# Performance work log

Hardware: AMD Instinct MI355X
Metric: run time of the kernel (lower is better)

Reference implementation:

```python
import jax, jax.numpy as jnp
import numpy as np

N_NODES = 200000
N_EDGES = 800000
N_GRAPHS = 4096
IN_FEAT = 64
CONV_SIZES = [128, 128, 256, 256]
MAX_DEGREE = 5  # buckets 0..5 (degree clamped)
N_CLASSES = 2


def setup_inputs() -> dict:
    key = jax.random.key(0)
    ks = jax.random.split(key, 32)
    inp = {}
    inp["x"] = jax.random.normal(ks[0], (N_NODES, IN_FEAT), dtype=jnp.float32)
    inp["edge_index"] = jax.random.randint(ks[1], (2, N_EDGES), 0, N_NODES, dtype=jnp.int32)
    inp["batch"] = jnp.sort(jax.random.randint(ks[2], (N_NODES,), 0, N_GRAPHS, dtype=jnp.int32))
    # per-layer MFConv params: Wl (neighbor-sum branch, with bias), Wr (root branch, no bias),
    # one linear per degree bucket -> leading dim MAX_DEGREE+1
    c_in = IN_FEAT
    k = 3
    for li, c_out in enumerate(CONV_SIZES):
        s = 1.0 / np.sqrt(c_in)
        inp[f"Wl{li}"] = jax.random.normal(ks[k], (MAX_DEGREE + 1, c_in, c_out), dtype=jnp.float32) * s; k += 1
        inp[f"bl{li}"] = jax.random.normal(ks[k], (MAX_DEGREE + 1, c_out), dtype=jnp.float32) * 0.01; k += 1
        inp[f"Wr{li}"] = jax.random.normal(ks[k], (MAX_DEGREE + 1, c_in, c_out), dtype=jnp.float32) * s; k += 1
        c_in = c_out
    in_final = sum(CONV_SIZES) + CONV_SIZES[-1]  # concat of all layer outputs + pooled last layer
    inp["Wf"] = jax.random.normal(ks[k], (in_final, N_CLASSES), dtype=jnp.float32) * (1.0 / np.sqrt(in_final)); k += 1
    inp["bf"] = jax.random.normal(ks[k], (N_CLASSES,), dtype=jnp.float32) * 0.01
    return inp


def _mfconv(x, src, dst, deg, Wl, bl, Wr):
    # neighbor sum aggregation (source_to_target flow): msg_i = sum_{j->i} x_j
    msg = jax.ops.segment_sum(x[src], dst, num_segments=x.shape[0])  # [N, c_in]
    out = jnp.zeros((x.shape[0], Wl.shape[2]), dtype=x.dtype)
    for d in range(Wl.shape[0]):  # small fixed loop over degree buckets
        r = msg @ Wl[d] + bl[d] + x @ Wr[d]
        out = jnp.where((deg == d)[:, None], r, out)
    return out


def reference(x, edge_index, batch,
              Wl0, bl0, Wr0, Wl1, bl1, Wr1, Wl2, bl2, Wr2, Wl3, bl3, Wr3,
              Wf, bf):
    src, dst = edge_index[0], edge_index[1]
    n = x.shape[0]
    deg = jnp.clip(jnp.zeros((n,), jnp.int32).at[dst].add(1), 0, MAX_DEGREE)
    hs = []
    h = x
    for Wl, bl, Wr in ((Wl0, bl0, Wr0), (Wl1, bl1, Wr1), (Wl2, bl2, Wr2), (Wl3, bl3, Wr3)):
        h = _mfconv(h, src, dst, deg, Wl, bl, Wr)
        hs.append(h)
    # global_add_pool then repeat_interleave back to nodes == gather pooled by batch id
    h_pool = jax.ops.segment_sum(h, batch, num_segments=N_GRAPHS)  # [G, c_last]
    h_pool_ = h_pool[batch]  # [N, c_last]
    h_cat = jnp.concatenate(hs + [h_pool_], axis=1)  # [N, sum(sizes)+c_last]
    logits = h_cat @ Wf + bf
    return jax.nn.softmax(logits, axis=1)
```

## Files before the change

### kernel.cpp

```cpp
#include <hip/hip_runtime.h>
#include <cstdint>
#include <cstddef>

namespace {

constexpr int NN   = 200000;
constexpr int NE   = 800000;
constexpr int NG   = 4096;
constexpr int MAXD = 5;

constexpr int BM = 64;
constexpr int KT = 32;
constexpr int NBC = (NN + 255) / 256;
constexpr int NBLK  = (NN + BM - 1) / BM + 6;
constexpr int PERMN = NBLK * BM;

typedef _Float16 half8 __attribute__((ext_vector_type(8)));
typedef _Float16 half4 __attribute__((ext_vector_type(4)));
typedef float    f32x4 __attribute__((ext_vector_type(4)));

constexpr size_t P_L0 = (size_t)6 * 128 * 128;
constexpr size_t P_L1 = (size_t)6 * 256 * 128;
constexpr size_t P_L2 = (size_t)6 * 256 * 256;
constexpr size_t P_L3 = (size_t)6 * 512 * 256;
constexpr size_t O_P0 = 0;
constexpr size_t O_P1 = O_P0 + P_L0;
constexpr size_t O_P2 = O_P1 + P_L1;
constexpr size_t O_P3 = O_P2 + P_L2;
constexpr size_t WTOT = O_P3 + P_L3;


__global__ void k_memset32(int* __restrict__ p, int v, int n) {
    int i = blockIdx.x * 256 + threadIdx.x;
    if (i < n) p[i] = v;
}

__global__ void k_report(float* __restrict__ outp, float v, int n) {
    int i = blockIdx.x * 256 + threadIdx.x;
    if (i < n) outp[i] = v;
}

template <int CIN, int COUT>
__global__ void k_wpack(const float* __restrict__ Wl, const float* __restrict__ Wr,
                        _Float16* __restrict__ hi, _Float16* __restrict__ lo) {
    constexpr int NT = CIN / 16;
    constexpr int NB = COUT / 16;
    const int total = 6 * NT * NB * 64;
    int idx = blockIdx.x * 256 + threadIdx.x;
    if (idx >= total) return;
    const int lane = idx & 63;
    int rest = idx >> 6;
    const int nb = rest % NB; rest /= NB;
    const int ti = rest % NT;
    const int d  = rest / NT;
    const int k0 = ti * 32 + ((lane >> 4) * 8);
    const int n  = nb * 16 + (lane & 15);
    half8 hv, lv;
#pragma unroll
    for (int j = 0; j < 8; j++) {
        const int kk = k0 + j;
        const float v = (kk < CIN)
                            ? Wl[((size_t)d * CIN + kk) * COUT + n]
                            : Wr[((size_t)d * CIN + (kk - CIN)) * COUT + n];
        const _Float16 h = (_Float16)v;
        hv[j] = h;
        lv[j] = (_Float16)(v - (float)h);
    }
    *(half8*)(hi + (size_t)idx * 8) = hv;
    *(half8*)(lo + (size_t)idx * 8) = lv;
}


__global__ void k_count_deg(const int* __restrict__ dst, int* __restrict__ deg) {
    int e = blockIdx.x * 256 + threadIdx.x;
    if (e < NE) atomicAdd(&deg[dst[e]], 1);
}

__global__ void k_scan_part(const int* __restrict__ deg, int* __restrict__ part) {
    __shared__ int s[256];
    int t = threadIdx.x, i = blockIdx.x * 256 + t;
    s[t] = (i < NN) ? deg[i] : 0;
    __syncthreads();
    for (int st = 128; st > 0; st >>= 1) {
        if (t < st) s[t] += s[t + st];
        __syncthreads();
    }
    if (t == 0) part[blockIdx.x] = s[0];
}

__global__ void k_scan_single(int* __restrict__ part, int nb) {
    __shared__ int s[1024];
    int t = threadIdx.x;
    int v0 = (t < nb) ? part[t] : 0;
    s[t] = v0;
    __syncthreads();
    for (int off = 1; off < 1024; off <<= 1) {
        int v = (t >= off) ? s[t - off] : 0;
        __syncthreads();
        s[t] += v;
        __syncthreads();
    }
    if (t < nb) part[t] = s[t] - v0;
}

__global__ void k_scan_final(const int* __restrict__ deg, const int* __restrict__ part,
                             int* __restrict__ row_ptr, int* __restrict__ cursor) {
    __shared__ int s[256];
    int t = threadIdx.x, i = blockIdx.x * 256 + t;
    int v0 = (i < NN) ? deg[i] : 0;
    s[t] = v0;
    __syncthreads();
    for (int off = 1; off < 256; off <<= 1) {
        int v = (t >= off) ? s[t - off] : 0;
        __syncthreads();
        s[t] += v;
        __syncthreads();
    }
    if (i < NN) {
        int excl = s[t] - v0 + part[blockIdx.x];
        row_ptr[i] = excl;
        cursor[i]  = excl;
        if (i == NN - 1) row_ptr[NN] = excl + v0;
    }
}

__global__ void k_fill_csr(const int* __restrict__ src, const int* __restrict__ dst,
                           int* __restrict__ cursor, int* __restrict__ col) {
    int e = blockIdx.x * 256 + threadIdx.x;
    if (e < NE) {
        int d = dst[e];
        int slot = atomicAdd(&cursor[d], 1);
        col[slot] = src[e];
    }
}


__global__ void k_bucket_blockcount(const int* __restrict__ deg, int* __restrict__ blkcnt) {
    __shared__ int h[6];
    int t = threadIdx.x;
    if (t < 6) h[t] = 0;
    __syncthreads();
    int i = blockIdx.x * 256 + t;
    if (i < NN) atomicAdd(&h[min(deg[i], MAXD)], 1);
    __syncthreads();
    if (t < 6) blkcnt[t * NBC + blockIdx.x] = h[t];
}

__global__ void k_bucket_scanall(int* __restrict__ blkcnt, int* __restrict__ bpad) {
    __shared__ int tot[6];
    int t = threadIdx.x;
    if (t < 6) {
        int run = 0;
        for (int j = 0; j < NBC; j++) {
            int v = blkcnt[t * NBC + j];
            blkcnt[t * NBC + j] = run;
            run += v;
        }
        tot[t] = run;
    }
    __syncthreads();
    if (t == 0) {
        int off = 0;
        for (int b = 0; b < 6; b++) {
            bpad[b] = off;
            off += ((tot[b] + BM - 1) / BM) * BM;
        }
        bpad[6] = off;
    }
}

__global__ void k_scatter2(const int* __restrict__ deg, const int* __restrict__ blkcnt,
                           const int* __restrict__ bpad, int* __restrict__ perm) {
    __shared__ int base[6];
    int t = threadIdx.x;
    if (t < 6) base[t] = bpad[t] + blkcnt[t * NBC + blockIdx.x];
    __syncthreads();
    int i = blockIdx.x * 256 + t;
    if (i < NN) {
        int b = min(deg[i], MAXD);
        int pos = atomicAdd(&base[b], 1);
        perm[pos] = i;
    }
}


__global__ void k_aggregate128(const float* __restrict__ hin, const int* __restrict__ row_ptr,
                               const int* __restrict__ col, float* __restrict__ msg) {
    int node = blockIdx.x * 4 + (threadIdx.x >> 6);
    int lane = threadIdx.x & 63;
    int s = row_ptr[node], e = row_ptr[node + 1];
    float2 acc = make_float2(0.f, 0.f);
    for (int p = s; p < e; p++) {
        const float2 v = *(const float2*)(hin + (size_t)col[p] * 128 + lane * 2);
        acc.x += v.x; acc.y += v.y;
    }
    *(float2*)(msg + (size_t)node * 128 + lane * 2) = acc;
}


template <int C0, int C1, int COUT, int BN_, bool POOL_FUSE>
__launch_bounds__(256, (BN_ == 256) ? 3 : 4)
__global__ void k_transform(const float* __restrict__ hin0, const float* __restrict__ hin1,
                            const int* __restrict__ row_ptr, const int* __restrict__ col,
                            const _Float16* __restrict__ wph, const _Float16* __restrict__ wpl,
                            const float* __restrict__ bias, const float* __restrict__ Wf,
                            const int* __restrict__ perm, const int* __restrict__ deg,
                            const int* __restrict__ batch,
                            float* __restrict__ out0, float* __restrict__ pool,
                            float* __restrict__ logits, int wf_off) {
    constexpr int CIN = C0 + C1;
    constexpr int NW0 = C0 / 32;
    constexpr int NW  = CIN / 32;
    constexpr int NT  = 2 * NW;
    constexpr int NB  = COUT / 16;
    constexpr int NTN = BN_ / 64;
    __shared__ _Float16 Ah[4][64][8];
    __shared__ _Float16 Al[4][64][8];
    __shared__ int rowid[BM];

    const int t  = threadIdx.x;
    const int m0 = blockIdx.x * BM;
    const int n0 = blockIdx.y * BN_;

    if (t < BM) rowid[t] = perm[m0 + t];
    __syncthreads();
    if (rowid[0] < 0) return;

    const int d = min(deg[rowid[0]], MAXD);

    const int am = t & 63, aq = t >> 6;
    const int anode = rowid[am];
    int es = 0, ee = 0;
    if (anode >= 0) { es = row_ptr[anode]; ee = row_ptr[anode + 1]; }
    const int lx = t & 15, qd = (t >> 4) & 3, wv = t >> 6;

    const int mt_w = am >> 4;
    const int lA1  = (am & 15) + ((aq >> 1) << 4);
    const int lA2  = (am & 15) + ((2 + (aq >> 1)) << 4);
    const int j0   = (aq & 1) * 4;

    const int nb0 = n0 / 16 + wv * NTN;

    auto gather = [&](int ti, float* g) {
#pragma unroll
        for (int i = 0; i < 8; i++) g[i] = 0.f;
        if (ti < NW) {
            const bool lo = (C1 == 0) || (ti < NW0);
            const float* base = lo ? hin0 : hin1;
            const int stride  = lo ? C0 : C1;
            const int off     = (lo ? 32 * ti : 32 * (ti - NW0)) + 4 * aq;
            for (int p = es; p < ee; p++) {
                const float* r = base + (size_t)col[p] * stride + off;
                const float4 a = *(const float4*)r;
                const float4 b = *(const float4*)(r + 16);
                g[0] += a.x; g[1] += a.y; g[2] += a.z; g[3] += a.w;
                g[4] += b.x; g[5] += b.y; g[6] += b.z; g[7] += b.w;
            }
        } else if (anode >= 0) {
            const int e = (ti - NW) * 32 + 4 * aq;
            const float* r = (C1 == 0 || e < C0)
                                 ? hin0 + (size_t)anode * C0 + e
                                 : hin1 + (size_t)anode * C1 + (e - C0);
            const float4 a = *(const float4*)r;
            const float4 b = *(const float4*)(r + 16);
            g[0] = a.x; g[1] = a.y; g[2] = a.z; g[3] = a.w;
            g[4] = b.x; g[5] = b.y; g[6] = b.z; g[7] = b.w;
        }
    };

    f32x4 acc[4][NTN];
#pragma unroll
    for (int mt = 0; mt < 4; mt++)
#pragma unroll
        for (int nt = 0; nt < NTN; nt++) acc[mt][nt] = (f32x4)0.f;

    float gcur[8];
    gather(0, gcur);

    for (int ti = 0; ti < NT; ti++) {
        {
            half4 h1, l1, h2, l2;
#pragma unroll
            for (int i = 0; i < 4; i++) {
                const _Float16 h = (_Float16)gcur[i];
                h1[i] = h; l1[i] = (_Float16)(gcur[i] - (float)h);
                const _Float16 g = (_Float16)gcur[4 + i];
                h2[i] = g; l2[i] = (_Float16)(gcur[4 + i] - (float)g);
            }
            *(half4*)&Ah[mt_w][lA1][j0] = h1;
            *(half4*)&Al[mt_w][lA1][j0] = l1;
            *(half4*)&Ah[mt_w][lA2][j0] = h2;
            *(half4*)&Al[mt_w][lA2][j0] = l2;
        }
        half8 bh[NTN], bl[NTN];
        {
            const size_t tbase = (((size_t)d * NT + ti) * NB) * 512;
#pragma unroll
            for (int nt = 0; nt < NTN; nt++) {
                const size_t off = tbase + (size_t)(nb0 + nt) * 512 + (size_t)am * 8;
                bh[nt] = *(const half8*)(wph + off);
                bl[nt] = *(const half8*)(wpl + off);
            }
        }
        __syncthreads();

        float gnext[8];
        if (ti + 1 < NT) {
            gather(ti + 1, gnext);
        } else {
#pragma unroll
            for (int i = 0; i < 8; i++) gnext[i] = 0.f;
        }

        {
            half8 ah[4], alo[4];
#pragma unroll
            for (int mt = 0; mt < 4; mt++) {
                ah[mt]  = *(const half8*)&Ah[mt][am][0];
                alo[mt] = *(const half8*)&Al[mt][am][0];
            }
#pragma unroll
            for (int nt = 0; nt < NTN; nt++)
#pragma unroll
                for (int mt = 0; mt < 4; mt++) {
                    acc[mt][nt] = __builtin_amdgcn_mfma_f32_16x16x32_f16(ah[mt],  bh[nt], acc[mt][nt], 0, 0, 0);
                    acc[mt][nt] = __builtin_amdgcn_mfma_f32_16x16x32_f16(alo[mt], bh[nt], acc[mt][nt], 0, 0, 0);
                    acc[mt][nt] = __builtin_amdgcn_mfma_f32_16x16x32_f16(ah[mt],  bl[nt], acc[mt][nt], 0, 0, 0);
                }
        }
        __syncthreads();

#pragma unroll
        for (int i = 0; i < 8; i++) gcur[i] = gnext[i];
    }

    float blv[NTN], w0[NTN], w1[NTN];
    int cols[NTN];
#pragma unroll
    for (int nt = 0; nt < NTN; nt++) {
        cols[nt] = n0 + wv * (16 * NTN) + nt * 16 + lx;
        blv[nt] = bias[d * COUT + cols[nt]];
        w0[nt]  = Wf[(size_t)(wf_off + cols[nt]) * 2 + 0];
        w1[nt]  = Wf[(size_t)(wf_off + cols[nt]) * 2 + 1];
    }
#pragma unroll
    for (int mt = 0; mt < 4; mt++)
#pragma unroll
    for (int r = 0; r < 4; r++) {
        const int node = rowid[mt * 16 + qd * 4 + r];
        float p0 = 0.f, p1 = 0.f;
        if (node >= 0) {
            float h[NTN];
#pragma unroll
            for (int nt = 0; nt < NTN; nt++) {
                h[nt] = acc[mt][nt][r] + blv[nt];
                p0 = fmaf(h[nt], w0[nt], p0);
                p1 = fmaf(h[nt], w1[nt], p1);
            }
            if constexpr (POOL_FUSE) {
                float* pr = pool + (size_t)batch[node] * 256;
#pragma unroll
                for (int nt = 0; nt < NTN; nt++) atomicAdd(&pr[cols[nt]], h[nt]);
            } else {
                float* orow = out0 + (size_t)node * COUT;
#pragma unroll
                for (int nt = 0; nt < NTN; nt++) orow[cols[nt]] = h[nt];
            }
        }
#pragma unroll
        for (int s = 1; s < 16; s <<= 1) {
            p0 += __shfl_xor(p0, s, 64);
            p1 += __shfl_xor(p1, s, 64);
        }
        if (node >= 0 && lx == 0) {
            atomicAdd(&logits[(size_t)node * 2 + 0], p0);
            atomicAdd(&logits[(size_t)node * 2 + 1], p1);
        }
    }
}


__launch_bounds__(256, 3)
__global__ void k_gemm2b(float* __restrict__ buf0, float* __restrict__ buf1,
                         const _Float16* __restrict__ wph, const _Float16* __restrict__ wpl,
                         const float* __restrict__ bias, const float* __restrict__ Wf,
                         const int* __restrict__ perm, const int* __restrict__ deg,
                         float* __restrict__ logits) {
    constexpr int COUT = 256, NT = 8, NB = 16, NTN = 4;
    __shared__ _Float16 Ah[4][64][8];
    __shared__ _Float16 Al[4][64][8];
    __shared__ int rowid[BM];

    const int t  = threadIdx.x;
    const int m0 = blockIdx.x * BM;

    if (t < BM) rowid[t] = perm[m0 + t];
    __syncthreads();
    if (rowid[0] < 0) return;

    const int d = min(deg[rowid[0]], MAXD);

    const int am = t & 63, aq = t >> 6;
    const int anode = rowid[am];
    const int lx = t & 15, qd = (t >> 4) & 3, wv = t >> 6;

    const int mt_w = am >> 4;
    const int lA1  = (am & 15) + ((aq >> 1) << 4);
    const int lA2  = (am & 15) + ((2 + (aq >> 1)) << 4);
    const int j0   = (aq & 1) * 4;
    const int nb0  = wv * NTN;

    f32x4 acc[4][NTN];
#pragma unroll
    for (int mt = 0; mt < 4; mt++)
#pragma unroll
        for (int nt = 0; nt < NTN; nt++) acc[mt][nt] = (f32x4)0.f;

    for (int ti = 0; ti < NT; ti++) {
        {
            const int gk0 = ti * 32 + 4 * aq;
            float4 v0 = make_float4(0.f, 0.f, 0.f, 0.f);
            float4 v1 = v0;
            if (anode >= 0) {
                const float* r = (gk0 < 128) ? buf0 + (size_t)anode * 128 + gk0
                                             : buf1 + (size_t)anode * 128 + (gk0 - 128);
                v0 = *(const float4*)r;
                v1 = *(const float4*)(r + 16);
            }
            const float g[8] = {v0.x, v0.y, v0.z, v0.w, v1.x, v1.y, v1.z, v1.w};
            half4 h1, l1, h2, l2;
#pragma unroll
            for (int i = 0; i < 4; i++) {
                const _Float16 h = (_Float16)g[i];
                h1[i] = h; l1[i] = (_Float16)(g[i] - (float)h);
                const _Float16 q = (_Float16)g[4 + i];
                h2[i] = q; l2[i] = (_Float16)(g[4 + i] - (float)q);
            }
            *(half4*)&Ah[mt_w][lA1][j0] = h1;
            *(half4*)&Al[mt_w][lA1][j0] = l1;
            *(half4*)&Ah[mt_w][lA2][j0] = h2;
            *(half4*)&Al[mt_w][lA2][j0] = l2;
        }
        half8 bh[NTN], bl[NTN];
        {
            const size_t tbase = (((size_t)d * NT + ti) * NB) * 512;
#pragma unroll
            for (int nt = 0; nt < NTN; nt++) {
                const size_t off = tbase + (size_t)(nb0 + nt) * 512 + (size_t)am * 8;
                bh[nt] = *(const half8*)(wph + off);
                bl[nt] = *(const half8*)(wpl + off);
            }
        }
        __syncthreads();
        {
            half8 ah[4], alo[4];
#pragma unroll
            for (int mt = 0; mt < 4; mt++) {
                ah[mt]  = *(const half8*)&Ah[mt][am][0];
                alo[mt] = *(const half8*)&Al[mt][am][0];
            }
#pragma unroll
            for (int nt = 0; nt < NTN; nt++)
#pragma unroll
                for (int mt = 0; mt < 4; mt++) {
                    acc[mt][nt] = __builtin_amdgcn_mfma_f32_16x16x32_f16(ah[mt],  bh[nt], acc[mt][nt], 0, 0, 0);
                    acc[mt][nt] = __builtin_amdgcn_mfma_f32_16x16x32_f16(alo[mt], bh[nt], acc[mt][nt], 0, 0, 0);
                    acc[mt][nt] = __builtin_amdgcn_mfma_f32_16x16x32_f16(ah[mt],  bl[nt], acc[mt][nt], 0, 0, 0);
                }
        }
        __syncthreads();
    }

    float blv[NTN], w0[NTN], w1[NTN];
    int cols[NTN];
#pragma unroll
    for (int nt = 0; nt < NTN; nt++) {
        cols[nt] = wv * 64 + nt * 16 + lx;
        blv[nt] = bias[d * COUT + cols[nt]];
        w0[nt]  = Wf[(size_t)(256 + cols[nt]) * 2 + 0];
        w1[nt]  = Wf[(size_t)(256 + cols[nt]) * 2 + 1];
    }
#pragma unroll
    for (int mt = 0; mt < 4; mt++)
#pragma unroll
    for (int r = 0; r < 4; r++) {
        const int node = rowid[mt * 16 + qd * 4 + r];
        float p0 = 0.f, p1 = 0.f;
        if (node >= 0) {
#pragma unroll
            for (int nt = 0; nt < NTN; nt++) {
                const float h = acc[mt][nt][r] + blv[nt];
                p0 = fmaf(h, w0[nt], p0);
                p1 = fmaf(h, w1[nt], p1);
                if (cols[nt] < 128) buf0[(size_t)node * 128 + cols[nt]] = h;
                else                buf1[(size_t)node * 128 + cols[nt] - 128] = h;
            }
        }
#pragma unroll
        for (int s = 1; s < 16; s <<= 1) {
            p0 += __shfl_xor(p0, s, 64);
            p1 += __shfl_xor(p1, s, 64);
        }
        if (node >= 0 && lx == 0) {
            atomicAdd(&logits[(size_t)node * 2 + 0], p0);
            atomicAdd(&logits[(size_t)node * 2 + 1], p1);
        }
    }
}


__global__ void k_pool_logits(const float* __restrict__ pool, const float* __restrict__ Wf,
                              const float* __restrict__ bf, float* __restrict__ pl) {
    int g = blockIdx.x * 4 + (threadIdx.x >> 6);
    int lane = threadIdx.x & 63;
    const float* pr = pool + (size_t)g * 256;
    float p0 = 0.f, p1 = 0.f;
#pragma unroll
    for (int j = 0; j < 4; j++) {
        int k = lane + 64 * j;
        float v = pr[k];
        p0 = fmaf(v, Wf[(size_t)(768 + k) * 2 + 0], p0);
        p1 = fmaf(v, Wf[(size_t)(768 + k) * 2 + 1], p1);
    }
#pragma unroll
    for (int s = 1; s < 64; s <<= 1) {
        p0 += __shfl_xor(p0, s, 64);
        p1 += __shfl_xor(p1, s, 64);
    }
    if (lane == 0) {
        pl[(size_t)g * 2 + 0] = p0 + bf[0];
        pl[(size_t)g * 2 + 1] = p1 + bf[1];
    }
}

__global__ void k_final(const float* __restrict__ logits, const float* __restrict__ pl,
                        const int* __restrict__ batch, float* __restrict__ outp) {
    int i = blockIdx.x * 256 + threadIdx.x;
    if (i < NN) {
        int g = batch[i];
        float l0 = logits[(size_t)i * 2 + 0] + pl[(size_t)g * 2 + 0];
        float l1 = logits[(size_t)i * 2 + 1] + pl[(size_t)g * 2 + 1];
        float m = fmaxf(l0, l1);
        float e0 = expf(l0 - m), e1 = expf(l1 - m);
        float inv = 1.f / (e0 + e1);
        outp[(size_t)i * 2 + 0] = e0 * inv;
        outp[(size_t)i * 2 + 1] = e1 * inv;
    }
}

}

extern "C" void kernel_launch(void* const* d_in, const int* in_sizes, int n_in,
                              void* d_out, int out_size, void* d_ws, size_t ws_size,
                              hipStream_t stream) {
    const float* x     = (const float*)d_in[0];
    const int*   ei    = (const int*)d_in[1];
    const int*   batch = (const int*)d_in[2];
    const float* Wl0 = (const float*)d_in[3];  const float* bl0 = (const float*)d_in[4];
    const float* Wr0 = (const float*)d_in[5];
    const float* Wl1 = (const float*)d_in[6];  const float* bl1 = (const float*)d_in[7];
    const float* Wr1 = (const float*)d_in[8];
    const float* Wl2 = (const float*)d_in[9];  const float* bl2 = (const float*)d_in[10];
    const float* Wr2 = (const float*)d_in[11];
    const float* Wl3 = (const float*)d_in[12]; const float* bl3 = (const float*)d_in[13];
    const float* Wr3 = (const float*)d_in[14];
    const float* Wf  = (const float*)d_in[15]; const float* bf  = (const float*)d_in[16];
    const int* src = ei;
    const int* dst = ei + NE;
    float* outp = (float*)d_out;
    (void)in_sizes; (void)n_in;

    char* w = (char*)d_ws;
    auto alloc = [&](size_t bytes) -> void* {
        void* p = (void*)w;
        w += (bytes + 255) & ~(size_t)255;
        return p;
    };
    int*   deg    = (int*)alloc((size_t)NN * 4);
    float* logits = (float*)alloc((size_t)NN * 2 * 4);
    float* pool   = (float*)alloc((size_t)NG * 256 * 4);
    size_t zero_words = (size_t)(w - (char*)deg) / 4;
    int*   bpad    = (int*)alloc(32);
    int*   blkcnt  = (int*)alloc((size_t)6 * NBC * 4);
    int*   perm    = (int*)alloc((size_t)PERMN * 4);
    int*   row_ptr = (int*)alloc((size_t)(NN + 1) * 4);
    int*   cursor  = (int*)alloc((size_t)NN * 4);
    int*   col     = (int*)alloc((size_t)NE * 4);
    int*   part    = (int*)alloc(1024 * 4);
    float* pl      = (float*)alloc((size_t)NG * 2 * 4);
    _Float16* whi  = (_Float16*)alloc(WTOT * 2);
    _Float16* wlo  = (_Float16*)alloc(WTOT * 2);
    float* bufA    = (float*)alloc((size_t)NN * 128 * 4);
    float* bufB    = (float*)alloc((size_t)NN * 128 * 4);

    size_t required = (size_t)(w - (char*)d_ws);
    if (required > ws_size) {
        k_report<<<(out_size + 255) / 256, 256, 0, stream>>>(
            outp, (float)(double)(ws_size >> 20), out_size);
        return;
    }

    dim3 b256(256);
    k_memset32<<<(int)((zero_words + 255) / 256), b256, 0, stream>>>((int*)deg, 0, (int)zero_words);
    k_memset32<<<(PERMN + 255) / 256, b256, 0, stream>>>(perm, -1, PERMN);

    k_wpack<64, 128><<<(int)(P_L0 / 8 + 255) / 256, b256, 0, stream>>>(Wl0, Wr0, whi + O_P0, wlo + O_P0);
    k_wpack<128, 128><<<(int)(P_L1 / 8 + 255) / 256, b256, 0, stream>>>(Wl1, Wr1, whi + O_P1, wlo + O_P1);
    k_wpack<128, 256><<<(int)(P_L2 / 8 + 255) / 256, b256, 0, stream>>>(Wl2, Wr2, whi + O_P2, wlo + O_P2);
    k_wpack<256, 256><<<(int)(P_L3 / 8 + 255) / 256, b256, 0, stream>>>(Wl3, Wr3, whi + O_P3, wlo + O_P3);

    k_count_deg<<<NE / 256, b256, 0, stream>>>(dst, deg);
    k_scan_part<<<NBC, b256, 0, stream>>>(deg, part);
    k_scan_single<<<1, 1024, 0, stream>>>(part, NBC);
    k_scan_final<<<NBC, b256, 0, stream>>>(deg, part, row_ptr, cursor);
    k_fill_csr<<<NE / 256, b256, 0, stream>>>(src, dst, cursor, col);
    k_bucket_blockcount<<<NBC, b256, 0, stream>>>(deg, blkcnt);
    k_bucket_scanall<<<1, 64, 0, stream>>>(blkcnt, bpad);
    k_scatter2<<<NBC, b256, 0, stream>>>(deg, blkcnt, bpad, perm);

    k_transform<64, 0, 128, 128, false><<<dim3(NBLK, 1), b256, 0, stream>>>(
        x, nullptr, row_ptr, col, whi + O_P0, wlo + O_P0,
        bl0, Wf, perm, deg, nullptr, bufA, nullptr, logits, 0);
    k_transform<128, 0, 128, 128, false><<<dim3(NBLK, 1), b256, 0, stream>>>(
        bufA, nullptr, row_ptr, col, whi + O_P1, wlo + O_P1,
        bl1, Wf, perm, deg, nullptr, bufB, nullptr, logits, 128);
    k_aggregate128<<<NN / 4, b256, 0, stream>>>(bufB, row_ptr, col, bufA);
    k_gemm2b<<<dim3(NBLK), b256, 0, stream>>>(
        bufA, bufB, whi + O_P2, wlo + O_P2, bl2, Wf, perm, deg, logits);
    k_transform<128, 128, 256, 256, true><<<dim3(NBLK, 1), b256, 0, stream>>>(
        bufA, bufB, row_ptr, col, whi + O_P3, wlo + O_P3,
        bl3, Wf, perm, deg, batch, nullptr, pool, logits, 512);

    k_pool_logits<<<NG / 4, b256, 0, stream>>>(pool, Wf, bf, pl);
    k_final<<<NBC, b256, 0, stream>>>(logits, pl, batch, outp);
}
```

Measured before the change: 1.486 ms.

## Stage full gathered A tile in LDS once and load root rows directly

The transform kernels now gather and sum the neighbor features for the whole input width in a single pass, each thread covering a contiguous quarter of the channels. The result is split into hi/lo fp16 and written into a full-K LDS tile behind one barrier, replacing the per-k-tile gather plus two syncs per iteration. The root-branch operand is read straight from global memory into MFMA register layout, with no LDS staging. The neighbor aggregation kernel is unrolled by two edges, and launch bounds drop to fewer waves per SIMD to make room for the larger LDS footprint and register use. The trade is lower occupancy and more LDS in exchange for fewer barriers and more memory-level parallelism in the gather.

```diff
diff --git a/kernel.cpp b/kernel.cpp
--- a/kernel.cpp
+++ b/kernel.cpp
@@ -10,7 +10,6 @@
 constexpr int MAXD = 5;
 
 constexpr int BM = 64;
-constexpr int KT = 32;
 constexpr int NBC = (NN + 255) / 256;
 constexpr int NBLK  = (NN + BM - 1) / BM + 6;
 constexpr int PERMN = NBLK * BM;
@@ -190,16 +189,23 @@
     int lane = threadIdx.x & 63;
     int s = row_ptr[node], e = row_ptr[node + 1];
     float2 acc = make_float2(0.f, 0.f);
-    for (int p = s; p < e; p++) {
+    int p = s;
+    for (; p + 2 <= e; p += 2) {
+        const int c0 = col[p], c1 = col[p + 1];
+        const float2 v0 = *(const float2*)(hin + (size_t)c0 * 128 + lane * 2);
+        const float2 v1 = *(const float2*)(hin + (size_t)c1 * 128 + lane * 2);
+        acc.x += v0.x + v1.x;
+        acc.y += v0.y + v1.y;
+    }
+    if (p < e) {
         const float2 v = *(const float2*)(hin + (size_t)col[p] * 128 + lane * 2);
         acc.x += v.x; acc.y += v.y;
     }
     *(float2*)(msg + (size_t)node * 128 + lane * 2) = acc;
 }
 
-
 template <int C0, int C1, int COUT, int BN_, bool POOL_FUSE>
-__launch_bounds__(256, (BN_ == 256) ? 3 : 4)
+__launch_bounds__(256, (C0 + C1 >= 256) ? 2 : 3)
 __global__ void k_transform(const float* __restrict__ hin0, const float* __restrict__ hin1,
                             const int* __restrict__ row_ptr, const int* __restrict__ col,
                             const _Float16* __restrict__ wph, const _Float16* __restrict__ wpl,
@@ -209,13 +215,15 @@
                             float* __restrict__ out0, float* __restrict__ pool,
                             float* __restrict__ logits, int wf_off) {
     constexpr int CIN = C0 + C1;
-    constexpr int NW0 = C0 / 32;
     constexpr int NW  = CIN / 32;
     constexpr int NT  = 2 * NW;
     constexpr int NB  = COUT / 16;
     constexpr int NTN = BN_ / 64;
-    __shared__ _Float16 Ah[4][64][8];
-    __shared__ _Float16 Al[4][64][8];
+    constexpr int CPT = CIN / 4;
+    constexpr int UQ  = CPT / 4;
+
+    __shared__ _Float16 Ah[NW][4][64][8];
+    __shared__ _Float16 Al[NW][4][64][8];
     __shared__ int rowid[BM];
 
     const int t  = threadIdx.x;
@@ -230,43 +238,49 @@
 
     const int am = t & 63, aq = t >> 6;
     const int anode = rowid[am];
-    int es = 0, ee = 0;
-    if (anode >= 0) { es = row_ptr[anode]; ee = row_ptr[anode + 1]; }
+
+    {
+        int es = 0, ee = 0;
+        if (anode >= 0) { es = row_ptr[anode]; ee = row_ptr[anode + 1]; }
+        const int k0 = CPT * aq;
+        const float* gsrc = (C1 == 0 || k0 < C0) ? hin0 : hin1;
+        const int    goff = (C1 == 0 || k0 < C0) ? k0 : (k0 - C0);
+
+        f32x4 acc[UQ];
+#pragma unroll
+        for (int u = 0; u < UQ; u++) acc[u] = (f32x4)0.f;
+        for (int p = es; p < ee; p++) {
+            const float* r = gsrc + (size_t)col[p] * C0 + goff;
+            f32x4 v[UQ];
+#pragma unroll
+            for (int u = 0; u < UQ; u++) v[u] = *(const f32x4*)(r + 4 * u);
+#pragma unroll
+            for (int u = 0; u < UQ; u++) acc[u] += v[u];
+        }
+        const int mt_w = am >> 4, rl = am & 15;
+#pragma unroll
+        for (int u = 0; u < UQ; u++) {
+            const int k  = k0 + 4 * u;
+            const int ti = k >> 5;
+            const int o  = (k >> 3) & 3;
+            const int j0 = k & 7;
+            half4 hv, lv;
+#pragma unroll
+            for (int i = 0; i < 4; i++) {
+                const _Float16 h = (_Float16)acc[u][i];
+                hv[i] = h; lv[i] = (_Float16)(acc[u][i] - (float)h);
+            }
+            *(half4*)&Ah[ti][mt_w][rl + 16 * o][j0] = hv;
+            *(half4*)&Al[ti][mt_w][rl + 16 * o][j0] = lv;
+        }
+    }
+    __syncthreads();
+
     const int lx = t & 15, qd = (t >> 4) & 3, wv = t >> 6;
-
-    const int mt_w = am >> 4;
-    const int lA1  = (am & 15) + ((aq >> 1) << 4);
-    const int lA2  = (am & 15) + ((2 + (aq >> 1)) << 4);
-    const int j0   = (aq & 1) * 4;
-
     const int nb0 = n0 / 16 + wv * NTN;
-
-    auto gather = [&](int ti, float* g) {
-#pragma unroll
-        for (int i = 0; i < 8; i++) g[i] = 0.f;
-        if (ti < NW) {
-            const bool lo = (C1 == 0) || (ti < NW0);
-            const float* base = lo ? hin0 : hin1;
-            const int stride  = lo ? C0 : C1;
-            const int off     = (lo ? 32 * ti : 32 * (ti - NW0)) + 4 * aq;
-            for (int p = es; p < ee; p++) {
-                const float* r = base + (size_t)col[p] * stride + off;
-                const float4 a = *(const float4*)r;
-                const float4 b = *(const float4*)(r + 16);
-                g[0] += a.x; g[1] += a.y; g[2] += a.z; g[3] += a.w;
-                g[4] += b.x; g[5] += b.y; g[6] += b.z; g[7] += b.w;
-            }
-        } else if (anode >= 0) {
-            const int e = (ti - NW) * 32 + 4 * aq;
-            const float* r = (C1 == 0 || e < C0)
-                                 ? hin0 + (size_t)anode * C0 + e
-                                 : hin1 + (size_t)anode * C1 + (e - C0);
-            const float4 a = *(const float4*)r;
-            const float4 b = *(const float4*)(r + 16);
-            g[0] = a.x; g[1] = a.y; g[2] = a.z; g[3] = a.w;
-            g[4] = b.x; g[5] = b.y; g[6] = b.z; g[7] = b.w;
-        }
-    };
+    int rnode[4];
+#pragma unroll
+    for (int mt = 0; mt < 4; mt++) rnode[mt] = rowid[(am & 15) + 16 * mt];
 
     f32x4 acc[4][NTN];
 #pragma unroll
@@ -274,64 +288,73 @@
 #pragma unroll
         for (int nt = 0; nt < NTN; nt++) acc[mt][nt] = (f32x4)0.f;
 
-    float gcur[8];
-    gather(0, gcur);
-
-    for (int ti = 0; ti < NT; ti++) {
-        {
-            half4 h1, l1, h2, l2;
+    for (int ti = 0; ti < NW; ti++) {
+        half8 bh[NTN], bl[NTN];
+        const size_t tbase = (((size_t)d * NT + ti) * NB) * 512;
+#pragma unroll
+        for (int nt = 0; nt < NTN; nt++) {
+            const size_t off = tbase + (size_t)(nb0 + nt) * 512 + (size_t)am * 8;
+            bh[nt] = *(const half8*)(wph + off);
+            bl[nt] = *(const half8*)(wpl + off);
+        }
+        half8 ah[4], alo[4];
+#pragma unroll
+        for (int mt = 0; mt < 4; mt++) {
+            ah[mt]  = *(const half8*)&Ah[ti][mt][am][0];
+            alo[mt] = *(const half8*)&Al[ti][mt][am][0];
+        }
+#pragma unroll
+        for (int nt = 0; nt < NTN; nt++)
+#pragma unroll
+            for (int mt = 0; mt < 4; mt++) {
+                acc[mt][nt] = __builtin_amdgcn_mfma_f32_16x16x32_f16(ah[mt],  bh[nt], acc[mt][nt], 0, 0, 0);
+                acc[mt][nt] = __builtin_amdgcn_mfma_f32_16x16x32_f16(alo[mt], bh[nt], acc[mt][nt], 0, 0, 0);
+                acc[mt][nt] = __builtin_amdgcn_mfma_f32_16x16x32_f16(ah[mt],  bl[nt], acc[mt][nt], 0, 0, 0);
+            }
+    }
+    for (int ti = NW; ti < NT; ti++) {
+        half8 bh[NTN], bl[NTN];
+        const size_t tbase = (((size_t)d * NT + ti) * NB) * 512;
+#pragma unroll
+        for (int nt = 0; nt < NTN; nt++) {
+            const size_t off = tbase + (size_t)(nb0 + nt) * 512 + (size_t)am * 8;
+            bh[nt] = *(const half8*)(wph + off);
+            bl[nt] = *(const half8*)(wpl + off);
+        }
+        const int e = (ti - NW) * 32 + 8 * (am >> 4);
+        f32x4 ra[4], rb[4];
+#pragma unroll
+        for (int mt = 0; mt < 4; mt++) {
+            ra[mt] = (f32x4)0.f; rb[mt] = (f32x4)0.f;
+            if (rnode[mt] >= 0) {
+                const float* r = (C1 == 0 || e < C0)
+                                     ? hin0 + (size_t)rnode[mt] * C0 + e
+                                     : hin1 + (size_t)rnode[mt] * C1 + (e - C0);
+                ra[mt] = *(const f32x4*)r;
+                rb[mt] = *(const f32x4*)(r + 4);
+            }
+        }
+        half8 ah[4], alo[4];
+#pragma unroll
+        for (int mt = 0; mt < 4; mt++) {
 #pragma unroll
             for (int i = 0; i < 4; i++) {
-                const _Float16 h = (_Float16)gcur[i];
-                h1[i] = h; l1[i] = (_Float16)(gcur[i] - (float)h);
-                const _Float16 g = (_Float16)gcur[4 + i];
-                h2[i] = g; l2[i] = (_Float16)(gcur[4 + i] - (float)g);
-            }
-            *(half4*)&Ah[mt_w][lA1][j0] = h1;
-            *(half4*)&Al[mt_w][lA1][j0] = l1;
-            *(half4*)&Ah[mt_w][lA2][j0] = h2;
-            *(half4*)&Al[mt_w][lA2][j0] = l2;
-        }
-        half8 bh[NTN], bl[NTN];
-        {
-            const size_t tbase = (((size_t)d * NT + ti) * NB) * 512;
-#pragma unroll
-            for (int nt = 0; nt < NTN; nt++) {
-                const size_t off = tbase + (size_t)(nb0 + nt) * 512 + (size_t)am * 8;
-                bh[nt] = *(const half8*)(wph + off);
-                bl[nt] = *(const half8*)(wpl + off);
-            }
-        }
-        __syncthreads();
-
-        float gnext[8];
-        if (ti + 1 < NT) {
-            gather(ti + 1, gnext);
-        } else {
-#pragma unroll
-            for (int i = 0; i < 8; i++) gnext[i] = 0.f;
-        }
-
-        {
-            half8 ah[4], alo[4];
+                const _Float16 h0 = (_Float16)ra[mt][i];
+                ah[mt][i] = h0;
+                alo[mt][i] = (_Float16)(ra[mt][i] - (float)h0);
+                const _Float16 h1 = (_Float16)rb[mt][i];
+                ah[mt][4 + i] = h1;
+                alo[mt][4 + i] = (_Float16)(rb[mt][i] - (float)h1);
+            }
+        }
+#pragma unroll
+        for (int nt = 0; nt < NTN; nt++)
 #pragma unroll
             for (int mt = 0; mt < 4; mt++) {
-                ah[mt]  = *(const half8*)&Ah[mt][am][0];
-                alo[mt] = *(const half8*)&Al[mt][am][0];
-            }
-#pragma unroll
-            for (int nt = 0; nt < NTN; nt++)
-#pragma unroll
-                for (int mt = 0; mt < 4; mt++) {
-                    acc[mt][nt] = __builtin_amdgcn_mfma_f32_16x16x32_f16(ah[mt],  bh[nt], acc[mt][nt], 0, 0, 0);
-                    acc[mt][nt] = __builtin_amdgcn_mfma_f32_16x16x32_f16(alo[mt], bh[nt], acc[mt][nt], 0, 0, 0);
-                    acc[mt][nt] = __builtin_amdgcn_mfma_f32_16x16x32_f16(ah[mt],  bl[nt], acc[mt][nt], 0, 0, 0);
-                }
-        }
-        __syncthreads();
-
-#pragma unroll
-        for (int i = 0; i < 8; i++) gcur[i] = gnext[i];
+                acc[mt][nt] = __builtin_amdgcn_mfma_f32_16x16x32_f16(ah[mt],  bh[nt], acc[mt][nt], 0, 0, 0);
+                acc[mt][nt] = __builtin_amdgcn_mfma_f32_16x16x32_f16(alo[mt], bh[nt], acc[mt][nt], 0, 0, 0);
+                acc[mt][nt] = __builtin_amdgcn_mfma_f32_16x16x32_f16(ah[mt],  bl[nt], acc[mt][nt], 0, 0, 0);
+            }
     }
 
     float blv[NTN], w0[NTN], w1[NTN];
@@ -380,15 +403,15 @@
 }
 
 
-__launch_bounds__(256, 3)
+__launch_bounds__(256, 2)
 __global__ void k_gemm2b(float* __restrict__ buf0, float* __restrict__ buf1,
                          const _Float16* __restrict__ wph, const _Float16* __restrict__ wpl,
                          const float* __restrict__ bias, const float* __restrict__ Wf,
                          const int* __restrict__ perm, const int* __restrict__ deg,
                          float* __restrict__ logits) {
     constexpr int COUT = 256, NT = 8, NB = 16, NTN = 4;
-    __shared__ _Float16 Ah[4][64][8];
-    __shared__ _Float16 Al[4][64][8];
+    __shared__ _Float16 Ah[NT][4][64][8];
+    __shared__ _Float16 Al[NT][4][64][8];
     __shared__ int rowid[BM];
 
     const int t  = threadIdx.x;
@@ -402,13 +425,39 @@
 
     const int am = t & 63, aq = t >> 6;
     const int anode = rowid[am];
+
+    {
+        const int k0 = 64 * aq;
+        f32x4 v[16];
+#pragma unroll
+        for (int u = 0; u < 16; u++) v[u] = (f32x4)0.f;
+        if (anode >= 0) {
+            const float* r = (aq < 2) ? buf0 + (size_t)anode * 128 + k0
+                                      : buf1 + (size_t)anode * 128 + (k0 - 128);
+#pragma unroll
+            for (int u = 0; u < 16; u++) v[u] = *(const f32x4*)(r + 4 * u);
+        }
+        const int mt_w = am >> 4, rl = am & 15;
+#pragma unroll
+        for (int u = 0; u < 16; u++) {
+            const int k  = k0 + 4 * u;
+            const int ti = k >> 5;
+            const int o  = (k >> 3) & 3;
+            const int j0 = k & 7;
+            half4 hv, lv;
+#pragma unroll
+            for (int i = 0; i < 4; i++) {
+                const _Float16 h = (_Float16)v[u][i];
+                hv[i] = h; lv[i] = (_Float16)(v[u][i] - (float)h);
+            }
+            *(half4*)&Ah[ti][mt_w][rl + 16 * o][j0] = hv;
+            *(half4*)&Al[ti][mt_w][rl + 16 * o][j0] = lv;
+        }
+    }
+    __syncthreads();
+
     const int lx = t & 15, qd = (t >> 4) & 3, wv = t >> 6;
-
-    const int mt_w = am >> 4;
-    const int lA1  = (am & 15) + ((aq >> 1) << 4);
-    const int lA2  = (am & 15) + ((2 + (aq >> 1)) << 4);
-    const int j0   = (aq & 1) * 4;
-    const int nb0  = wv * NTN;
+    const int nb0 = wv * NTN;
 
     f32x4 acc[4][NTN];
 #pragma unroll
@@ -417,58 +466,28 @@
         for (int nt = 0; nt < NTN; nt++) acc[mt][nt] = (f32x4)0.f;
 
     for (int ti = 0; ti < NT; ti++) {
-        {
-            const int gk0 = ti * 32 + 4 * aq;
-            float4 v0 = make_float4(0.f, 0.f, 0.f, 0.f);
-            float4 v1 = v0;
-            if (anode >= 0) {
-                const float* r = (gk0 < 128) ? buf0 + (size_t)anode * 128 + gk0
-                                             : buf1 + (size_t)anode * 128 + (gk0 - 128);
-                v0 = *(const float4*)r;
-                v1 = *(const float4*)(r + 16);
-            }
-            const float g[8] = {v0.x, v0.y, v0.z, v0.w, v1.x, v1.y, v1.z, v1.w};
-            half4 h1, l1, h2, l2;
-#pragma unroll
-            for (int i = 0; i < 4; i++) {
-                const _Float16 h = (_Float16)g[i];
-                h1[i] = h; l1[i] = (_Float16)(g[i] - (float)h);
-                const _Float16 q = (_Float16)g[4 + i];
-                h2[i] = q; l2[i] = (_Float16)(g[4 + i] - (float)q);
-            }
-            *(half4*)&Ah[mt_w][lA1][j0] = h1;
-            *(half4*)&Al[mt_w][lA1][j0] = l1;
-            *(half4*)&Ah[mt_w][lA2][j0] = h2;
-            *(half4*)&Al[mt_w][lA2][j0] = l2;
-        }
         half8 bh[NTN], bl[NTN];
-        {
-            const size_t tbase = (((size_t)d * NT + ti) * NB) * 512;
-#pragma unroll
-            for (int nt = 0; nt < NTN; nt++) {
-                const size_t off = tbase + (size_t)(nb0 + nt) * 512 + (size_t)am * 8;
-                bh[nt] = *(const half8*)(wph + off);
-                bl[nt] = *(const half8*)(wpl + off);
-            }
-        }
-        __syncthreads();
-        {
-            half8 ah[4], alo[4];
+        const size_t tbase = (((size_t)d * NT + ti) * NB) * 512;
+#pragma unroll
+        for (int nt = 0; nt < NTN; nt++) {
+            const size_t off = tbase + (size_t)(nb0 + nt) * 512 + (size_t)am * 8;
+            bh[nt] = *(const half8*)(wph + off);
+            bl[nt] = *(const half8*)(wpl + off);
+        }
+        half8 ah[4], alo[4];
+#pragma unroll
+        for (int mt = 0; mt < 4; mt++) {
+            ah[mt]  = *(const half8*)&Ah[ti][mt][am][0];
+            alo[mt] = *(const half8*)&Al[ti][mt][am][0];
+        }
+#pragma unroll
+        for (int nt = 0; nt < NTN; nt++)
 #pragma unroll
             for (int mt = 0; mt < 4; mt++) {
-                ah[mt]  = *(const half8*)&Ah[mt][am][0];
-                alo[mt] = *(const half8*)&Al[mt][am][0];
-            }
-#pragma unroll
-            for (int nt = 0; nt < NTN; nt++)
-#pragma unroll
-                for (int mt = 0; mt < 4; mt++) {
-                    acc[mt][nt] = __builtin_amdgcn_mfma_f32_16x16x32_f16(ah[mt],  bh[nt], acc[mt][nt], 0, 0, 0);
-                    acc[mt][nt] = __builtin_amdgcn_mfma_f32_16x16x32_f16(alo[mt], bh[nt], acc[mt][nt], 0, 0, 0);
-                    acc[mt][nt] = __builtin_amdgcn_mfma_f32_16x16x32_f16(ah[mt],  bl[nt], acc[mt][nt], 0, 0, 0);
-                }
-        }
-        __syncthreads();
+                acc[mt][nt] = __builtin_amdgcn_mfma_f32_16x16x32_f16(ah[mt],  bh[nt], acc[mt][nt], 0, 0, 0);
+                acc[mt][nt] = __builtin_amdgcn_mfma_f32_16x16x32_f16(alo[mt], bh[nt], acc[mt][nt], 0, 0, 0);
+                acc[mt][nt] = __builtin_amdgcn_mfma_f32_16x16x32_f16(ah[mt],  bl[nt], acc[mt][nt], 0, 0, 0);
+            }
     }
 
     float blv[NTN], w0[NTN], w1[NTN];
```

Result: slower. 1.573 ms (+5.8%).
